# Optimization experiments

Measured on AMD Instinct MI355X. Metric: run time of the kernel, lower is better.

The kernel has to match this reference:

```python
import jax, jax.numpy as jnp
import numpy as np

B, N, DIM, H, DH = 4, 2048, 512, 8, 64
INNER = H * DH  # 512
SCALE = DH ** -0.5


def setup_inputs() -> dict:
    key = jax.random.key(0)
    k1, k2, k3, k4 = jax.random.split(key, 4)
    x = jax.random.normal(k1, (B, N, DIM), dtype=jnp.float32)
    bias = jax.random.normal(k2, (B, N, DIM), dtype=jnp.float32)
    # to_qkv: Linear(dim, inner*3, bias=False)
    w_qkv = jax.random.normal(k3, (DIM, 3 * INNER), dtype=jnp.float32) * (DIM ** -0.5)
    # to_out: Linear(inner, dim) with bias (project_out=True since heads != 1)
    w_out = jax.random.normal(k4, (INNER, DIM), dtype=jnp.float32) * (INNER ** -0.5)
    b_out = jnp.zeros((DIM,), dtype=jnp.float32)
    return {"x": x, "bias": bias, "w_qkv": w_qkv, "w_out": w_out, "b_out": b_out}


def _split_heads(t):
    # [b, n, h*d] -> [b, h, n, d]
    b, n, _ = t.shape
    return t.reshape(b, n, H, DH).transpose(0, 2, 1, 3)


def reference(x, bias, w_qkv, w_out, b_out):
    qkv = x @ w_qkv  # [b, n, 3*inner]
    q, k, v = jnp.split(qkv, 3, axis=-1)
    q, k, v = map(_split_heads, (q, k, v))
    dots = jnp.einsum('bhid,bhjd->bhij', q, k) * SCALE  # [b,h,n,n]

    qkv_b = bias @ w_qkv
    qb, kb, _ = jnp.split(qkv_b, 3, axis=-1)
    qb, kb = _split_heads(qb), _split_heads(kb)
    dots = dots + jnp.einsum('bhid,bhjd->bhij', qb, kb) * SCALE

    attn = jax.nn.softmax(dots, axis=-1)
    out = jnp.einsum('bhij,bhjd->bhid', attn, v)  # [b,h,n,d]
    out = out.transpose(0, 2, 1, 3).reshape(x.shape[0], x.shape[1], INNER)
    return out @ w_out + b_out
```

## Files before the change

### kernel.cpp

```cpp
#include <hip/hip_runtime.h>
#include <hip/hip_bf16.h>

#define DEV __device__ __forceinline__

typedef __attribute__((ext_vector_type(8))) short short8;
typedef __attribute__((ext_vector_type(4))) int i32x4;
typedef __attribute__((ext_vector_type(2))) int i32x2;
typedef __attribute__((ext_vector_type(4))) float f32x4;
typedef __attribute__((ext_vector_type(16))) float f32x16;

constexpr int B = 4, N = 2048, H = 8, DH = 64;
constexpr int INNER = H * DH;
constexpr int BH = B * H;
constexpr float QSCALE = 0.125f * 1.44269504088896f;

constexpr size_t OFF_WQKVT = 0;
constexpr size_t OFF_WOUTT = OFF_WQKVT + (size_t)1536 * 512;
constexpr size_t OFF_QT    = OFF_WOUTT + (size_t)512 * 512;
constexpr size_t OFF_KT    = OFF_QT + (size_t)BH * N * 128;
constexpr size_t OFF_VT    = OFF_KT + (size_t)BH * N * 128;
constexpr size_t OFF_AO    = OFF_VT + (size_t)BH * DH * N;
constexpr size_t OFF_XBF   = OFF_AO + (size_t)8192 * 512;
constexpr size_t OFF_BBF   = OFF_AO;

DEV short f2b(float f) {
    __hip_bfloat16 h = __float2bfloat16(f);
    return __builtin_bit_cast(short, h);
}

DEV int cvtpk(float lo, float hi) {
    int r;
    asm("v_cvt_pk_bf16_f32 %0, %1, %2" : "=v"(r) : "v"(lo), "v"(hi));
    return r;
}

DEV float fexp2(float x) {
    float r;
    asm("v_exp_f32 %0, %1" : "=v"(r) : "v"(x));
    return r;
}

DEV void plswap(int& a, int& b) {
    i32x2 r = __builtin_amdgcn_permlane32_swap(a, b, false, false);
    a = r.x; b = r.y;
}

DEV void gload16(const void* g, void* l) {
    __builtin_amdgcn_global_load_lds(
        (const __attribute__((address_space(1))) unsigned int*)g,
        (__attribute__((address_space(3))) unsigned int*)l, 16, 0, 0);
}

__global__ void prep_kernel(const float* __restrict__ wqkv,
                            const float* __restrict__ wout,
                            const float* __restrict__ x,
                            const float* __restrict__ bias,
                            __hip_bfloat16* __restrict__ ws) {
    __hip_bfloat16* wqkvT = ws + OFF_WQKVT;
    __hip_bfloat16* woutT = ws + OFF_WOUTT;
    short8* xbf = (short8*)(ws + OFF_XBF);
    short8* bbf = (short8*)(ws + OFF_BBF);
    int tid = blockIdx.x * blockDim.x + threadIdx.x;
    const int nconv = 8192 * 512 / 8;
    const int t1 = 512 * 1536 / 4;
    const int t2 = 512 * 512 / 4;
    const int total = 2 * nconv + t1 + t2;
    for (int i = tid; i < total; i += gridDim.x * blockDim.x) {
        if (i < 2 * nconv) {
            const float4* src = (const float4*)(i < nconv ? x : bias);
            short8* dst = i < nconv ? xbf : bbf;
            int j = i < nconv ? i : i - nconv;
            float4 v0 = src[2 * j], v1 = src[2 * j + 1];
            short8 sv;
            sv[0] = f2b(v0.x); sv[1] = f2b(v0.y); sv[2] = f2b(v0.z); sv[3] = f2b(v0.w);
            sv[4] = f2b(v1.x); sv[5] = f2b(v1.y); sv[6] = f2b(v1.z); sv[7] = f2b(v1.w);
            dst[j] = sv;
        } else if (i < 2 * nconv + t1) {
            int j = i - 2 * nconv;
            int k  = j / 384;
            int c4 = (j % 384) * 4;
            float4 v = ((const float4*)wqkv)[j];
            wqkvT[(size_t)(c4 + 0) * 512 + k] = __float2bfloat16(v.x);
            wqkvT[(size_t)(c4 + 1) * 512 + k] = __float2bfloat16(v.y);
            wqkvT[(size_t)(c4 + 2) * 512 + k] = __float2bfloat16(v.z);
            wqkvT[(size_t)(c4 + 3) * 512 + k] = __float2bfloat16(v.w);
        } else {
            int j = i - 2 * nconv - t1;
            int k  = j / 128;
            int c4 = (j % 128) * 4;
            float4 v = ((const float4*)wout)[j];
            woutT[(size_t)(c4 + 0) * 512 + k] = __float2bfloat16(v.x);
            woutT[(size_t)(c4 + 1) * 512 + k] = __float2bfloat16(v.y);
            woutT[(size_t)(c4 + 2) * 512 + k] = __float2bfloat16(v.z);
            woutT[(size_t)(c4 + 3) * 512 + k] = __float2bfloat16(v.w);
        }
    }
}

__global__ __launch_bounds__(256) void gemm_qkv(__hip_bfloat16* __restrict__ ws) {
    int mt = blockIdx.x, yt = blockIdx.y;
    bool src_is_bias = (yt >= 12);
    int nt = src_is_bias ? yt - 12 : yt;
    const short* A  = (const short*)(ws + (src_is_bias ? OFF_BBF : OFF_XBF));
    const short* Bt = (const short*)(ws + OFF_WQKVT);
    int m0 = mt * 128, n0 = nt * 128;
    bool isV = (!src_is_bias && nt >= 8);

    __shared__ __align__(16) short As[128][64];
    __shared__ __align__(16) short Bs[128][64];

    int tid  = threadIdx.x;
    int wave = tid >> 6, lane = tid & 63;
    int wrow = wave >> 1, wcol = wave & 1;
    int lg = lane >> 4, li = lane & 15;

    f32x4 acc[4][4] = {};

    auto kloop = [&](bool swp) {
        for (int k0 = 0; k0 < 512; k0 += 64) {
#pragma unroll
            for (int i = 0; i < 4; ++i) {
                int c = wave * 4 + i;
                int r = c * 8 + (lane >> 3);
                gload16((const char*)A + ((size_t)(m0 + r) * 512 + k0 + (lane & 7) * 8) * 2,
                        (char*)&As[0][0] + c * 1024);
                gload16((const char*)Bt + ((size_t)(n0 + r) * 512 + k0 + (lane & 7) * 8) * 2,
                        (char*)&Bs[0][0] + c * 1024);
            }
            __syncthreads();
#pragma unroll
            for (int ks = 0; ks < 2; ++ks) {
                short8 af[4], bf[4];
#pragma unroll
                for (int m = 0; m < 4; ++m)
                    af[m] = *(const short8*)(&As[wrow * 64 + m * 16 + li][ks * 32 + lg * 8]);
#pragma unroll
                for (int n = 0; n < 4; ++n)
                    bf[n] = *(const short8*)(&Bs[wcol * 64 + n * 16 + li][ks * 32 + lg * 8]);
#pragma unroll
                for (int m = 0; m < 4; ++m)
#pragma unroll
                    for (int n = 0; n < 4; ++n)
                        acc[m][n] = swp
                            ? __builtin_amdgcn_mfma_f32_16x16x32_bf16(bf[n], af[m], acc[m][n], 0, 0, 0)
                            : __builtin_amdgcn_mfma_f32_16x16x32_bf16(af[m], bf[n], acc[m][n], 0, 0, 0);
            }
            __syncthreads();
        }
    };
    if (isV) kloop(false); else kloop(true);

    __hip_bfloat16* QT = ws + OFF_QT;
    __hip_bfloat16* KT = ws + OFF_KT;
    __hip_bfloat16* VT = ws + OFF_VT;

    if (isV) {
        int cc_base = n0 - 1024 + wcol * 64;
#pragma unroll
        for (int m = 0; m < 4; ++m) {
            int row0 = m0 + wrow * 64 + m * 16 + lg * 4;
            int b = row0 >> 11, nn = row0 & 2047;
#pragma unroll
            for (int n = 0; n < 4; ++n) {
                int cc = cc_base + n * 16 + li;
                int h = cc >> 6, d = cc & 63;
                int w0 = cvtpk(acc[m][n][0], acc[m][n][1]);
                int w1 = cvtpk(acc[m][n][2], acc[m][n][3]);
                short* p = (short*)VT + (size_t)((b * H + h) * DH + d) * N + nn;
                i32x2 wv = { w0, w1 };
                *(i32x2*)p = wv;
            }
        }
    } else {
        int qkoff = src_is_bias ? 64 : 0;
        bool isQ = (n0 < 512);
#pragma unroll
        for (int m = 0; m < 4; ++m) {
            int row = m0 + wrow * 64 + m * 16 + li;
            int b = row >> 11, nn = row & 2047;
#pragma unroll
            for (int n = 0; n < 4; ++n) {
                int cc0 = n0 + wcol * 64 + n * 16 + lg * 4;
                int w0, w1;
                short* p;
                if (isQ) {
                    int h = cc0 >> 6, d0 = (cc0 & 63) + qkoff;
                    w0 = cvtpk(acc[m][n][0] * QSCALE, acc[m][n][1] * QSCALE);
                    w1 = cvtpk(acc[m][n][2] * QSCALE, acc[m][n][3] * QSCALE);
                    p = (short*)QT + ((size_t)(b * H + h) * N + nn) * 128 + d0;
                } else {
                    int c = cc0 - 512;
                    int h = c >> 6, d0 = (c & 63) + qkoff;
                    w0 = cvtpk(acc[m][n][0], acc[m][n][1]);
                    w1 = cvtpk(acc[m][n][2], acc[m][n][3]);
                    p = (short*)KT + ((size_t)(b * H + h) * N + nn) * 128 + d0;
                }
                i32x2 wv = { w0, w1 };
                *(i32x2*)p = wv;
            }
        }
    }
}

__global__ __launch_bounds__(256, 3) void attn_kernel(__hip_bfloat16* __restrict__ ws) {
    int bid = blockIdx.x;
    int c   = bid & 7;
    int idx = bid >> 3;
    int bh  = (idx & 3) * 8 + c;
    int qb  = idx >> 2;

    int wave = threadIdx.x >> 6, lane = threadIdx.x & 63;
    int li32 = lane & 31, hi = lane >> 5;
    int qr0 = qb * 128 + wave * 32;

    const short* QT  = (const short*)(ws + OFF_QT) + (size_t)bh * N * 128;
    const char*  KTg = (const char*)((const short*)(ws + OFF_KT) + (size_t)bh * N * 128);
    const char*  VTg = (const char*)((const short*)(ws + OFF_VT) + (size_t)bh * DH * N);

    __shared__ __align__(16) short Ktile[2][64][128];
    __shared__ __align__(16) short Vtile[2][64][64];

    short8 qf[8];
#pragma unroll
    for (int kc = 0; kc < 8; ++kc)
        qf[kc] = *(const short8*)(QT + (size_t)(qr0 + li32) * 128 + kc * 16 + hi * 8);

    float m_run = -3e38f, l_run = 0.f;
    f32x16 o[2] = {};

    auto stage = [&](int t, int b) {
        int kv0 = t * 64;
#pragma unroll
        for (int cc = 0; cc < 4; ++cc) {
            int ck = wave * 4 + cc;
            int r  = ck * 4 + (lane >> 4);
            int cbx = (lane & 15) * 16;
            gload16(KTg + (size_t)(kv0 + r) * 256 + (cbx ^ ((r & 7) << 4)),
                    (char*)&Ktile[b][0][0] + ck * 1024);
        }
#pragma unroll
        for (int cc = 0; cc < 2; ++cc) {
            int ck = wave * 2 + cc;
            int r  = ck * 8 + (lane >> 3);
            int cbx = (lane & 7) * 16;
            gload16(VTg + (size_t)r * 4096 + kv0 * 2 + (cbx ^ ((r & 7) << 4)),
                    (char*)&Vtile[b][0][0] + ck * 1024);
        }
    };

    const char* Kb0 = (const char*)&Ktile[0][0][0];
    const char* Kb1 = (const char*)&Ktile[1][0][0];
    const char* Vb0 = (const char*)&Vtile[0][0][0];
    const char* Vb1 = (const char*)&Vtile[1][0][0];

    auto tile = [&](const char* Kb, const char* Vb) {
        f32x16 sT[2] = {};
        __builtin_amdgcn_s_setprio(1);
#pragma unroll
        for (int sub = 0; sub < 2; ++sub) {
            int row = sub * 32 + li32;
            int sw  = (row & 7) << 4;
            const char* kbase = Kb + row * 256;
#pragma unroll
            for (int kc = 0; kc < 8; ++kc) {
                short8 kf = *(const short8*)(kbase + ((kc * 32 + hi * 16) ^ sw));
                sT[sub] = __builtin_amdgcn_mfma_f32_32x32x16_bf16(kf, qf[kc], sT[sub], 0, 0, 0);
            }
        }
        __builtin_amdgcn_s_setprio(0);

        float t0[8];
#pragma unroll
        for (int j = 0; j < 8; ++j)
            t0[j] = fmaxf(fmaxf(sT[0][j], sT[0][j + 8]), fmaxf(sT[1][j], sT[1][j + 8]));
        float pm = fmaxf(fmaxf(fmaxf(t0[0], t0[1]), fmaxf(t0[2], t0[3])),
                         fmaxf(fmaxf(t0[4], t0[5]), fmaxf(t0[6], t0[7])));
        pm = fmaxf(pm, __shfl_xor(pm, 32));

        if (__any(pm > m_run + 8.f)) {
            float mn = fmaxf(m_run, pm);
            float al = fexp2(m_run - mn);
#pragma unroll
            for (int a = 0; a < 2; ++a)
#pragma unroll
                for (int r = 0; r < 16; ++r) o[a][r] *= al;
            l_run *= al;
            m_run = mn;
        }

        float lsp[4] = {0.f, 0.f, 0.f, 0.f};
        int w[2][8];
#pragma unroll
        for (int sub = 0; sub < 2; ++sub)
#pragma unroll
            for (int r2 = 0; r2 < 8; ++r2) {
                float p0 = fexp2(sT[sub][2 * r2]     - m_run);
                float p1 = fexp2(sT[sub][2 * r2 + 1] - m_run);
                lsp[r2 & 3] += p0 + p1;
                w[sub][r2] = cvtpk(p0, p1);
            }
        l_run += (lsp[0] + lsp[1]) + (lsp[2] + lsp[3]);

        short8 pf[2][2];
#pragma unroll
        for (int sub = 0; sub < 2; ++sub) {
            plswap(w[sub][0], w[sub][2]); plswap(w[sub][1], w[sub][3]);
            plswap(w[sub][4], w[sub][6]); plswap(w[sub][5], w[sub][7]);
            i32x4 f0 = { w[sub][0], w[sub][1], w[sub][2], w[sub][3] };
            i32x4 f1 = { w[sub][4], w[sub][5], w[sub][6], w[sub][7] };
            pf[sub][0] = __builtin_bit_cast(short8, f0);
            pf[sub][1] = __builtin_bit_cast(short8, f1);
        }

        __builtin_amdgcn_s_setprio(1);
#pragma unroll
        for (int sub = 0; sub < 2; ++sub)
#pragma unroll
            for (int ksel = 0; ksel < 2; ++ksel) {
                int cc = sub * 2 + ksel;
#pragma unroll
                for (int a = 0; a < 2; ++a) {
                    int row = a * 32 + li32;
                    int sw  = (row & 7) << 4;
                    short8 vf = *(const short8*)(Vb + row * 128 + ((cc * 32 + hi * 16) ^ sw));
                    o[a] = __builtin_amdgcn_mfma_f32_32x32x16_bf16(vf, pf[sub][ksel], o[a], 0, 0, 0);
                }
            }
        __builtin_amdgcn_s_setprio(0);

        __syncthreads();
    };

    stage(0, 0);
    __syncthreads();

    for (int t = 0; t < 32; t += 2) {
        stage(t + 1, 1);
        tile(Kb0, Vb0);
        if (t + 2 < 32) stage(t + 2, 0);
        tile(Kb1, Vb1);
    }

    l_run += __shfl_xor(l_run, 32);
    __hip_bfloat16* AO = ws + OFF_AO;
    int b = bh >> 3, h = bh & 7;
    char* tb = (char*)&Ktile[0][0][0] + wave * 4096;
    float inv = 1.f / l_run;
#pragma unroll
    for (int a = 0; a < 2; ++a)
#pragma unroll
        for (int r2 = 0; r2 < 8; ++r2) {
            int r = 2 * r2;
            int dv = (r & 3) + 8 * (r >> 2) + 4 * hi + 32 * a;
            int word = cvtpk(o[a][r] * inv, o[a][r + 1] * inv);
            *(int*)(tb + li32 * 128 + ((dv * 2) ^ ((li32 & 7) << 4))) = word;
        }
#pragma unroll
    for (int qq = 0; qq < 32; qq += 8) {
        int q = qq + (lane >> 3), seg = lane & 7;
        short8 vrow = *(const short8*)(tb + q * 128 + ((seg * 16) ^ ((q & 7) << 4)));
        *(short8*)(AO + (size_t)(b * N + qr0 + q) * INNER + h * 64 + seg * 8) = vrow;
    }
}

__global__ __launch_bounds__(256) void gemm_out(const __hip_bfloat16* __restrict__ ws_c,
                                                const float* __restrict__ bout,
                                                float* __restrict__ out) {
    const short* AO = (const short*)(ws_c + OFF_AO);
    const short* Bt = (const short*)(ws_c + OFF_WOUTT);
    int m0 = blockIdx.x * 128, n0 = blockIdx.y * 128;

    __shared__ __align__(16) short As[128][64];
    __shared__ __align__(16) short Bs[128][64];

    int tid  = threadIdx.x;
    int wave = tid >> 6, lane = tid & 63;
    int wrow = wave >> 1, wcol = wave & 1;
    int lg = lane >> 4, li = lane & 15;

    f32x4 acc[4][4] = {};

    for (int k0 = 0; k0 < 512; k0 += 64) {
#pragma unroll
        for (int i = 0; i < 4; ++i) {
            int c = wave * 4 + i;
            int r = c * 8 + (lane >> 3);
            gload16((const char*)AO + ((size_t)(m0 + r) * 512 + k0 + (lane & 7) * 8) * 2,
                    (char*)&As[0][0] + c * 1024);
            gload16((const char*)Bt + ((size_t)(n0 + r) * 512 + k0 + (lane & 7) * 8) * 2,
                    (char*)&Bs[0][0] + c * 1024);
        }
        __syncthreads();
#pragma unroll
        for (int ks = 0; ks < 2; ++ks) {
            short8 af[4], bf[4];
#pragma unroll
            for (int m = 0; m < 4; ++m)
                af[m] = *(const short8*)(&As[wrow * 64 + m * 16 + li][ks * 32 + lg * 8]);
#pragma unroll
            for (int n = 0; n < 4; ++n)
                bf[n] = *(const short8*)(&Bs[wcol * 64 + n * 16 + li][ks * 32 + lg * 8]);
#pragma unroll
            for (int m = 0; m < 4; ++m)
#pragma unroll
                for (int n = 0; n < 4; ++n)
                    acc[m][n] = __builtin_amdgcn_mfma_f32_16x16x32_bf16(bf[n], af[m], acc[m][n], 0, 0, 0);
        }
        __syncthreads();
    }

    float4 bb[4];
#pragma unroll
    for (int n = 0; n < 4; ++n)
        bb[n] = *(const float4*)(bout + n0 + wcol * 64 + n * 16 + lg * 4);
#pragma unroll
    for (int m = 0; m < 4; ++m) {
        int row = m0 + wrow * 64 + m * 16 + li;
#pragma unroll
        for (int n = 0; n < 4; ++n) {
            int c0 = n0 + wcol * 64 + n * 16 + lg * 4;
            float4 v = { acc[m][n][0] + bb[n].x, acc[m][n][1] + bb[n].y,
                         acc[m][n][2] + bb[n].z, acc[m][n][3] + bb[n].w };
            *(float4*)(out + (size_t)row * 512 + c0) = v;
        }
    }
}

extern "C" void kernel_launch(void* const* d_in, const int* in_sizes, int n_in,
                              void* d_out, int out_size, void* d_ws, size_t ws_size,
                              hipStream_t stream) {
    const float* x    = (const float*)d_in[0];
    const float* bias = (const float*)d_in[1];
    const float* wqkv = (const float*)d_in[2];
    const float* wout = (const float*)d_in[3];
    const float* bout = (const float*)d_in[4];
    float* out = (float*)d_out;
    __hip_bfloat16* ws = (__hip_bfloat16*)d_ws;

    hipLaunchKernelGGL(prep_kernel, dim3(2048), dim3(256), 0, stream, wqkv, wout, x, bias, ws);
    hipLaunchKernelGGL(gemm_qkv, dim3(64, 20), dim3(256), 0, stream, ws);
    hipLaunchKernelGGL(attn_kernel, dim3(512), dim3(256), 0, stream, ws);
    hipLaunchKernelGGL(gemm_out, dim3(64, 4), dim3(256), 0, stream, (const __hip_bfloat16*)ws, bout, out);
}
```

Measured before the change: 139.1 us.

## Triple-buffer K/V tiles in attention with one barrier per tile

Switches the attention kernel's K/V shared-memory staging from double to triple buffering. Each tile now waits on vmcnt so only the current tile's async loads have landed, then passes a single barrier before issuing the load two tiles ahead. The per-tile trailing __syncthreads is removed. The cost is 50% more LDS per block and launch bounds lowered from 3 to 2 blocks per CU, which trades occupancy for deeper prefetch.

After: 140.8 us. About the same (+1.2%).

```diff
diff --git a/kernel.cpp b/kernel.cpp
--- a/kernel.cpp
+++ b/kernel.cpp
@@ -202,7 +202,7 @@
     }
 }
 
-__global__ __launch_bounds__(256, 3) void attn_kernel(__hip_bfloat16* __restrict__ ws) {
+__global__ __launch_bounds__(256, 2) void attn_kernel(__hip_bfloat16* __restrict__ ws) {
     int bid = blockIdx.x;
     int c   = bid & 7;
     int idx = bid >> 3;
@@ -217,8 +217,8 @@
     const char*  KTg = (const char*)((const short*)(ws + OFF_KT) + (size_t)bh * N * 128);
     const char*  VTg = (const char*)((const short*)(ws + OFF_VT) + (size_t)bh * DH * N);
 
-    __shared__ __align__(16) short Ktile[2][64][128];
-    __shared__ __align__(16) short Vtile[2][64][64];
+    __shared__ __align__(16) short Ktile[3][64][128];
+    __shared__ __align__(16) short Vtile[3][64][64];
 
     short8 qf[8];
 #pragma unroll
@@ -228,32 +228,30 @@
     float m_run = -3e38f, l_run = 0.f;
     f32x16 o[2] = {};
 
-    auto stage = [&](int t, int b) {
+    auto stage = [&](int t, int bsel) {
         int kv0 = t * 64;
+        char* Kd = (char*)&Ktile[0][0][0] + bsel * 16384;
+        char* Vd = (char*)&Vtile[0][0][0] + bsel * 8192;
 #pragma unroll
         for (int cc = 0; cc < 4; ++cc) {
             int ck = wave * 4 + cc;
             int r  = ck * 4 + (lane >> 4);
             int cbx = (lane & 15) * 16;
-            gload16(KTg + (size_t)(kv0 + r) * 256 + (cbx ^ ((r & 7) << 4)),
-                    (char*)&Ktile[b][0][0] + ck * 1024);
+            gload16(KTg + (size_t)(kv0 + r) * 256 + (cbx ^ ((r & 7) << 4)), Kd + ck * 1024);
         }
 #pragma unroll
         for (int cc = 0; cc < 2; ++cc) {
             int ck = wave * 2 + cc;
             int r  = ck * 8 + (lane >> 3);
             int cbx = (lane & 7) * 16;
-            gload16(VTg + (size_t)r * 4096 + kv0 * 2 + (cbx ^ ((r & 7) << 4)),
-                    (char*)&Vtile[b][0][0] + ck * 1024);
+            gload16(VTg + (size_t)r * 4096 + kv0 * 2 + (cbx ^ ((r & 7) << 4)), Vd + ck * 1024);
         }
     };
 
-    const char* Kb0 = (const char*)&Ktile[0][0][0];
-    const char* Kb1 = (const char*)&Ktile[1][0][0];
-    const char* Vb0 = (const char*)&Vtile[0][0][0];
-    const char* Vb1 = (const char*)&Vtile[1][0][0];
-
-    auto tile = [&](const char* Kb, const char* Vb) {
+    auto tile = [&](int bsel) {
+        const char* Kb = (const char*)&Ktile[0][0][0] + bsel * 16384;
+        const char* Vb = (const char*)&Vtile[0][0][0] + bsel * 8192;
+
         f32x16 sT[2] = {};
         __builtin_amdgcn_s_setprio(1);
 #pragma unroll
@@ -327,18 +325,23 @@
                 }
             }
         __builtin_amdgcn_s_setprio(0);
-
-        __syncthreads();
     };
 
     stage(0, 0);
-    __syncthreads();
-
-    for (int t = 0; t < 32; t += 2) {
-        stage(t + 1, 1);
-        tile(Kb0, Vb0);
-        if (t + 2 < 32) stage(t + 2, 0);
-        tile(Kb1, Vb1);
+    stage(1, 1);
+
+    int bsel = 0;
+    for (int t = 0; t < 32; ++t) {
+        if (t < 31) asm volatile("s_waitcnt vmcnt(6)" ::: "memory");
+        else        asm volatile("s_waitcnt vmcnt(0)" ::: "memory");
+        __builtin_amdgcn_s_barrier();
+        __builtin_amdgcn_sched_barrier(0);
+        if (t + 2 < 32) {
+            int b2 = bsel + 2 >= 3 ? bsel - 1 : bsel + 2;
+            stage(t + 2, b2);
+        }
+        tile(bsel);
+        bsel = bsel + 1 >= 3 ? 0 : bsel + 1;
     }
 
     l_run += __shfl_xor(l_run, 32);
```

## Triple-buffer QKV GEMM k-loop with async prefetch two stages ahead

Applied to the files above, without the earlier changes.

Replaces the single-buffered 64-wide k-loop in the QKV projection GEMM with a 3-stage ring of 32-wide k-tiles. Global-to-LDS loads run two iterations ahead and are ordered with explicit vmcnt waits and a single barrier per step, so load latency overlaps with MFMA work. Launch bounds now request 3 blocks per CU. The risks are register pressure from the occupancy hint and halved MFMA work per barrier. Correctness depends on the hand-written waitcnt counts matching the number of outstanding loads.

Result: slower. 146.3 us (+5.2%).

```diff
diff --git a/kernel.cpp b/kernel.cpp
--- a/kernel.cpp
+++ b/kernel.cpp
@@ -97,7 +97,7 @@
     }
 }
 
-__global__ __launch_bounds__(256) void gemm_qkv(__hip_bfloat16* __restrict__ ws) {
+__global__ __launch_bounds__(256, 3) void gemm_qkv(__hip_bfloat16* __restrict__ ws) {
     int mt = blockIdx.x, yt = blockIdx.y;
     bool src_is_bias = (yt >= 12);
     int nt = src_is_bias ? yt - 12 : yt;
@@ -106,8 +106,8 @@
     int m0 = mt * 128, n0 = nt * 128;
     bool isV = (!src_is_bias && nt >= 8);
 
-    __shared__ __align__(16) short As[128][64];
-    __shared__ __align__(16) short Bs[128][64];
+    __shared__ __align__(16) short As[3][128][32];
+    __shared__ __align__(16) short Bs[3][128][32];
 
     int tid  = threadIdx.x;
     int wave = tid >> 6, lane = tid & 63;
@@ -116,39 +116,53 @@
 
     f32x4 acc[4][4] = {};
 
-    auto kloop = [&](bool swp) {
-        for (int k0 = 0; k0 < 512; k0 += 64) {
-#pragma unroll
-            for (int i = 0; i < 4; ++i) {
-                int c = wave * 4 + i;
-                int r = c * 8 + (lane >> 3);
-                gload16((const char*)A + ((size_t)(m0 + r) * 512 + k0 + (lane & 7) * 8) * 2,
-                        (char*)&As[0][0] + c * 1024);
-                gload16((const char*)Bt + ((size_t)(n0 + r) * 512 + k0 + (lane & 7) * 8) * 2,
-                        (char*)&Bs[0][0] + c * 1024);
-            }
-            __syncthreads();
-#pragma unroll
-            for (int ks = 0; ks < 2; ++ks) {
-                short8 af[4], bf[4];
-#pragma unroll
-                for (int m = 0; m < 4; ++m)
-                    af[m] = *(const short8*)(&As[wrow * 64 + m * 16 + li][ks * 32 + lg * 8]);
-#pragma unroll
-                for (int n = 0; n < 4; ++n)
-                    bf[n] = *(const short8*)(&Bs[wcol * 64 + n * 16 + li][ks * 32 + lg * 8]);
-#pragma unroll
-                for (int m = 0; m < 4; ++m)
-#pragma unroll
-                    for (int n = 0; n < 4; ++n)
-                        acc[m][n] = swp
-                            ? __builtin_amdgcn_mfma_f32_16x16x32_bf16(bf[n], af[m], acc[m][n], 0, 0, 0)
-                            : __builtin_amdgcn_mfma_f32_16x16x32_bf16(af[m], bf[n], acc[m][n], 0, 0, 0);
-            }
-            __syncthreads();
+    auto stage = [&](int t, int bsel) {
+        int k0 = t * 32;
+#pragma unroll
+        for (int i = 0; i < 2; ++i) {
+            int ck = wave * 2 + i;
+            int r  = ck * 16 + (lane >> 2);
+            int cb = (lane & 3) * 8;
+            gload16((const char*)A + ((size_t)(m0 + r) * 512 + k0 + cb) * 2,
+                    (char*)&As[bsel][0][0] + ck * 1024);
+            gload16((const char*)Bt + ((size_t)(n0 + r) * 512 + k0 + cb) * 2,
+                    (char*)&Bs[bsel][0][0] + ck * 1024);
         }
     };
-    if (isV) kloop(false); else kloop(true);
+
+    auto compute = [&](int bsel, bool swp) {
+        short8 af[4], bf[4];
+#pragma unroll
+        for (int m = 0; m < 4; ++m)
+            af[m] = *(const short8*)(&As[bsel][wrow * 64 + m * 16 + li][lg * 8]);
+#pragma unroll
+        for (int n = 0; n < 4; ++n)
+            bf[n] = *(const short8*)(&Bs[bsel][wcol * 64 + n * 16 + li][lg * 8]);
+#pragma unroll
+        for (int m = 0; m < 4; ++m)
+#pragma unroll
+            for (int n = 0; n < 4; ++n)
+                acc[m][n] = swp
+                    ? __builtin_amdgcn_mfma_f32_16x16x32_bf16(bf[n], af[m], acc[m][n], 0, 0, 0)
+                    : __builtin_amdgcn_mfma_f32_16x16x32_bf16(af[m], bf[n], acc[m][n], 0, 0, 0);
+    };
+
+    stage(0, 0);
+    stage(1, 1);
+
+    int bsel = 0;
+    for (int t = 0; t < 16; ++t) {
+        if (t < 15) asm volatile("s_waitcnt vmcnt(4)" ::: "memory");
+        else        asm volatile("s_waitcnt vmcnt(0)" ::: "memory");
+        __builtin_amdgcn_s_barrier();
+        __builtin_amdgcn_sched_barrier(0);
+        if (t + 2 < 16) {
+            int b2 = bsel + 2 >= 3 ? bsel - 1 : bsel + 2;
+            stage(t + 2, b2);
+        }
+        if (isV) compute(bsel, false); else compute(bsel, true);
+        bsel = bsel + 1 >= 3 ? 0 : bsel + 1;
+    }
 
     __hip_bfloat16* QT = ws + OFF_QT;
     __hip_bfloat16* KT = ws + OFF_KT;
```
